# Kernel tuning notes

Measured on AMD Instinct MI355X. Metric: run time of the kernel, lower is better.

## Reference

```python
import jax, jax.numpy as jnp
import numpy as np

ALPHA = 0.5


def _chamfer(a, b):
    # Equivalent math to cKDTree k=1 queries: exact nearest-neighbor distances
    # between the two flattened clouds, computed brute-force.
    a = a.reshape(-1, 3)
    b = b.reshape(-1, 3)
    d2 = (jnp.sum(a * a, axis=1)[:, None]
          + jnp.sum(b * b, axis=1)[None, :]
          - 2.0 * (a @ b.T))                      # [Na, Nb]
    d = jnp.sqrt(jnp.clip(d2, 0.0))
    dist1 = jnp.min(d, axis=0)   # tree1(a).query(b): NN dist of each b point
    dist2 = jnp.min(d, axis=1)   # tree2(b).query(a): NN dist of each a point
    return jnp.mean(dist1) + jnp.mean(dist2)


def _pairwise_distances(x, y):
    # x: [B,N,3], y: [B,M,3] -> [B,N,M] euclidean distances (clamped-sqrt trick)
    x2 = jnp.sum(x * x, axis=-1, keepdims=True)            # [B,N,1]
    y2 = jnp.sum(y * y, axis=-1, keepdims=True)            # [B,M,1]
    d2 = x2 + jnp.swapaxes(y2, 2, 1) - 2.0 * jnp.einsum('bnd,bmd->bnm', x, y)
    return jnp.sqrt(jnp.clip(d2, 0.0))


def _confidence_scores(input_pcd, gt_pcd):
    # Faithful to torch.norm on the broadcast difference: [B,P,M,3] -> [B,P,M]
    diff = input_pcd[:, :, None, :] - gt_pcd[:, None, :, :]
    dist = jnp.linalg.norm(diff, axis=-1)
    min_d = jnp.min(dist, axis=-1)                         # [B,P]
    return jnp.exp(-min_d)[..., None]                      # [B,P,1]


def setup_inputs() -> dict:
    key = jax.random.key(0)
    k0, k1, k2, k3, k4 = jax.random.split(key, 5)
    B, N, M, P, NS = 4, 2048, 2048, 2048, 1024
    return {
        'pc1_0': jax.random.normal(k0, (B, N, 3), dtype=jnp.float32),
        'pc1_1': jax.random.normal(k1, (B, NS, 3), dtype=jnp.float32),
        'pc1_3': jax.random.uniform(k2, (B, P, 1), dtype=jnp.float32),
        'pc2': jax.random.normal(k3, (B, M, 3), dtype=jnp.float32),
        'pc3': jax.random.normal(k4, (B, P, 3), dtype=jnp.float32),
    }


def reference(pc1_0, pc1_1, pc1_3, pc2, pc3):
    # ChamferDistance detaches inputs in torch (cpu/numpy path) -> stop_gradient
    cd = jax.lax.stop_gradient(_chamfer(pc1_0, pc2))
    # In the original, emd_dist is immediately overwritten by pairwise_distances
    emd_dist = _pairwise_distances(pc1_0, pc2)             # [B,N,M]
    gt_scores = _confidence_scores(pc3, pc2)               # [B,P,1]
    confidence_loss = jnp.mean((pc1_3 - gt_scores) ** 2)
    seed_loss = jax.lax.stop_gradient(_chamfer(pc1_1, pc2))
    upsampling_loss = ALPHA * cd + (1.0 - ALPHA) * emd_dist
    final_loss = confidence_loss + upsampling_loss + seed_loss  # broadcasts to [B,N,M]
    return final_loss
```

## Files before the change

### kernel.cpp

```cpp
#include <hip/hip_runtime.h>
#include <math.h>


constexpr int OUT_TOTAL  = 4 * 2048 * 2048;
constexpr int PART_TOTAL = 416 * 2048;
constexpr int PART_OFS   = OUT_TOTAL - PART_TOTAL;

typedef float nfloat4 __attribute__((ext_vector_type(4)));

__global__ __launch_bounds__(256) void nn_kernel(
    const float* __restrict__ A0,
    const float* __restrict__ A1,
    const float* __restrict__ P2,
    const float* __restrict__ P3,
    float* __restrict__ part)
{
    __shared__ float4 lds[256];
    int bid = blockIdx.x;
    const float* A; const float* Bp; int at; int btile;
    if (bid < 128)      { int l = bid;       A = A0; Bp = P2; at = l >> 5; btile = l & 31; }
    else if (bid < 256) { int l = bid - 128; A = P2; Bp = A0; at = l >> 5; btile = l & 31; }
    else if (bid < 320) { int l = bid - 256; A = A1; Bp = P2; at = l >> 5; btile = l & 31; }
    else if (bid < 384) { int l = bid - 320; A = P2; Bp = A1; at = l >> 4; btile = l & 15; }
    else { int l = bid - 384; int b = l >> 3; btile = l & 7; at = 0;
           A = P3 + b * 6144; Bp = P2 + b * 6144; }

    {
        const float* s = Bp + (btile * 256 + threadIdx.x) * 3;
        float bx = s[0], by = s[1], bz = s[2];
        float nb2 = -0.5f * fmaf(bx, bx, fmaf(by, by, bz * bz));
        lds[threadIdx.x] = make_float4(bx, by, bz, nb2);
    }

    int a_base = at * 2048 + threadIdx.x * 8;
    const float4* av = (const float4*)(A + a_base * 3);
    float4 v0 = av[0], v1 = av[1], v2 = av[2], v3 = av[3], v4 = av[4], v5 = av[5];
    float ax[8], ay[8], az[8], a2[8], mx[8];
    ax[0]=v0.x; ay[0]=v0.y; az[0]=v0.z;
    ax[1]=v0.w; ay[1]=v1.x; az[1]=v1.y;
    ax[2]=v1.z; ay[2]=v1.w; az[2]=v2.x;
    ax[3]=v2.y; ay[3]=v2.z; az[3]=v2.w;
    ax[4]=v3.x; ay[4]=v3.y; az[4]=v3.z;
    ax[5]=v3.w; ay[5]=v4.x; az[5]=v4.y;
    ax[6]=v4.z; ay[6]=v4.w; az[6]=v5.x;
    ax[7]=v5.y; ay[7]=v5.z; az[7]=v5.w;
    #pragma unroll
    for (int k = 0; k < 8; k++) {
        a2[k] = fmaf(ax[k], ax[k], fmaf(ay[k], ay[k], az[k]*az[k]));
        mx[k] = -3.4e38f;
    }
    __syncthreads();

    #pragma unroll 4
    for (int j = 0; j < 256; j++) {
        float4 b = lds[j];
        #pragma unroll
        for (int k = 0; k < 8; k++) {
            float u = fmaf(az[k], b.z, b.w);
            u = fmaf(ay[k], b.y, u);
            u = fmaf(ax[k], b.x, u);
            mx[k] = fmaxf(mx[k], u);
        }
    }
    float4 o0, o1;
    o0.x = fmaxf(fmaf(-2.f, mx[0], a2[0]), 0.f);
    o0.y = fmaxf(fmaf(-2.f, mx[1], a2[1]), 0.f);
    o0.z = fmaxf(fmaf(-2.f, mx[2], a2[2]), 0.f);
    o0.w = fmaxf(fmaf(-2.f, mx[3], a2[3]), 0.f);
    o1.x = fmaxf(fmaf(-2.f, mx[4], a2[4]), 0.f);
    o1.y = fmaxf(fmaf(-2.f, mx[5], a2[5]), 0.f);
    o1.z = fmaxf(fmaf(-2.f, mx[6], a2[6]), 0.f);
    o1.w = fmaxf(fmaf(-2.f, mx[7], a2[7]), 0.f);
    float4* op = (float4*)(part + bid * 2048 + threadIdx.x * 8);
    op[0] = o0;
    op[1] = o1;
}

__global__ __launch_bounds__(1024) void reduce_kernel(
    const float* __restrict__ part,
    const float* __restrict__ conf_in,
    float* __restrict__ ws)
{
    int g = blockIdx.x;
    int tid = threadIdx.x;
    int base, bt; float scale; bool isconf = false;
    if (g < 8)       { int at = g >> 1;            base = (at * 32) * 2048       + (g & 1) * 1024; bt = 32; scale = 0.5f / 8192.f; }
    else if (g < 16) { int l = g - 8;  int at = l >> 1; base = (128 + at * 32) * 2048 + (l & 1) * 1024; bt = 32; scale = 0.5f / 8192.f; }
    else if (g < 20) { int l = g - 16; int at = l >> 1; base = (256 + at * 32) * 2048 + (l & 1) * 1024; bt = 32; scale = 1.f / 4096.f; }
    else if (g < 28) { int l = g - 20; int at = l >> 1; base = (320 + at * 16) * 2048 + (l & 1) * 1024; bt = 16; scale = 1.f / 8192.f; }
    else             { int l = g - 28; int b = l >> 1;  base = (384 + b * 8) * 2048   + (l & 1) * 1024; bt = 8;  scale = 1.f / 8192.f; isconf = true; }

    float m = 3.4e38f;
    const float* p = part + base + tid;
    #pragma unroll 4
    for (int t = 0; t < bt; t++, p += 2048) m = fminf(m, p[0]);
    float d = sqrtf(m);
    float sum;
    if (!isconf) {
        sum = d;
    } else {
        float e = conf_in[(g - 28) * 1024 + tid] - __expf(-d);
        sum = e * e;
    }
    #pragma unroll
    for (int ofs = 32; ofs > 0; ofs >>= 1) sum += __shfl_down(sum, ofs);
    __shared__ float red[16];
    if ((tid & 63) == 0) red[tid >> 6] = sum;
    __syncthreads();
    if (tid == 0) {
        float tot = 0.f;
        #pragma unroll
        for (int i = 0; i < 16; i++) tot += red[i];
        ws[g] = tot * scale;
    }
}

__global__ __launch_bounds__(256) void out_kernel(
    const float* __restrict__ pc1_0,
    const float* __restrict__ pc2,
    const float* __restrict__ wsp,
    float* __restrict__ out)
{
    int blk = blockIdx.x;
    int batch = blk >> 8;
    int n8 = blk & 255;
    int tid = threadIdx.x;
    float S = 0.f;
    #pragma unroll
    for (int t = 0; t < 36; t++) S += wsp[t];
    const float* bb = pc2 + batch * 6144;
    float bx[8], by[8], bz[8];
    {
        const float4* p = (const float4*)(bb + tid * 12);
        float4 u0 = p[0], u1 = p[1], u2 = p[2];
        bx[0]=u0.x; by[0]=u0.y; bz[0]=u0.z;
        bx[1]=u0.w; by[1]=u1.x; bz[1]=u1.y;
        bx[2]=u1.z; by[2]=u1.w; bz[2]=u2.x;
        bx[3]=u2.y; by[3]=u2.z; bz[3]=u2.w;
    }
    {
        const float4* p = (const float4*)(bb + 3072 + tid * 12);
        float4 u0 = p[0], u1 = p[1], u2 = p[2];
        bx[4]=u0.x; by[4]=u0.y; bz[4]=u0.z;
        bx[5]=u0.w; by[5]=u1.x; bz[5]=u1.y;
        bx[6]=u1.z; by[6]=u1.w; bz[6]=u2.x;
        bx[7]=u2.y; by[7]=u2.z; bz[7]=u2.w;
    }
    const float* arow = pc1_0 + batch * 6144 + n8 * 24;
    float* ob = out + (long)((batch << 11) + (n8 << 3)) * 2048 + tid * 4;
    #pragma unroll
    for (int r = 0; r < 8; r++) {
        float axx = arow[r*3], ayy = arow[r*3+1], azz = arow[r*3+2];
        float o[8];
        #pragma unroll
        for (int k = 0; k < 8; k++) {
            float dx = axx - bx[k], dy = ayy - by[k], dz = azz - bz[k];
            float d2 = fmaf(dx, dx, fmaf(dy, dy, dz*dz));
            o[k] = fmaf(0.5f, sqrtf(d2), S);
        }
        nfloat4 lo = { o[0], o[1], o[2], o[3] };
        nfloat4 hi = { o[4], o[5], o[6], o[7] };
        __builtin_nontemporal_store(lo, (nfloat4*)(ob + r * 2048));
        __builtin_nontemporal_store(hi, (nfloat4*)(ob + r * 2048 + 1024));
    }
}

extern "C" void kernel_launch(void* const* d_in, const int* in_sizes, int n_in,
                              void* d_out, int out_size, void* d_ws, size_t ws_size,
                              hipStream_t stream) {
    const float* pc1_0 = (const float*)d_in[0];
    const float* pc1_1 = (const float*)d_in[1];
    const float* pc1_3 = (const float*)d_in[2];
    const float* pc2   = (const float*)d_in[3];
    const float* pc3   = (const float*)d_in[4];
    float* out = (float*)d_out;
    float* ws  = (float*)d_ws;
    float* part = out + PART_OFS;

    nn_kernel<<<416, 256, 0, stream>>>(pc1_0, pc1_1, pc2, pc3, part);
    reduce_kernel<<<36, 1024, 0, stream>>>(part, pc1_3, ws);
    out_kernel<<<1024, 256, 0, stream>>>(pc1_0, pc2, ws, out);
}
```

Before: 112.2 us.

## Use fp16 dot2 for nearest-neighbor search and split work over more blocks

The x,y coordinates of both point clouds are packed into fp16 pairs so each candidate distance takes one v_dot2 instruction plus one FMA instead of three FMAs. Each thread now handles 2 query points instead of 8, so the grid grows from 416 to 1664 blocks, and the partial-minimum layout and reduce indexing are changed to match. The aim is more parallelism across the GPU and fewer instructions per distance. The cost is lower precision in the nearest-neighbor distances, which could break tolerance, plus more LDS reads per useful FMA.

```diff
diff --git a/kernel.cpp b/kernel.cpp
--- a/kernel.cpp
+++ b/kernel.cpp
@@ -3,10 +3,16 @@
 
 
 constexpr int OUT_TOTAL  = 4 * 2048 * 2048;
-constexpr int PART_TOTAL = 416 * 2048;
+constexpr int PART_TOTAL = 1664 * 512;
 constexpr int PART_OFS   = OUT_TOTAL - PART_TOTAL;
 
 typedef float nfloat4 __attribute__((ext_vector_type(4)));
+typedef _Float16 h2 __attribute__((ext_vector_type(2)));
+
+static __device__ __forceinline__ float pack2h(float x, float y) {
+    h2 v; v[0] = (_Float16)x; v[1] = (_Float16)y;
+    return __builtin_bit_cast(float, v);
+}
 
 __global__ __launch_bounds__(256) void nn_kernel(
     const float* __restrict__ A0,
@@ -18,62 +24,47 @@
     __shared__ float4 lds[256];
     int bid = blockIdx.x;
     const float* A; const float* Bp; int at; int btile;
-    if (bid < 128)      { int l = bid;       A = A0; Bp = P2; at = l >> 5; btile = l & 31; }
-    else if (bid < 256) { int l = bid - 128; A = P2; Bp = A0; at = l >> 5; btile = l & 31; }
-    else if (bid < 320) { int l = bid - 256; A = A1; Bp = P2; at = l >> 5; btile = l & 31; }
-    else if (bid < 384) { int l = bid - 320; A = P2; Bp = A1; at = l >> 4; btile = l & 15; }
-    else { int l = bid - 384; int b = l >> 3; btile = l & 7; at = 0;
+    if (bid < 512)       { int l = bid;        A = A0; Bp = P2; at = l >> 5; btile = l & 31; }
+    else if (bid < 1024) { int l = bid - 512;  A = P2; Bp = A0; at = l >> 5; btile = l & 31; }
+    else if (bid < 1280) { int l = bid - 1024; A = A1; Bp = P2; at = l >> 5; btile = l & 31; }
+    else if (bid < 1536) { int l = bid - 1280; A = P2; Bp = A1; at = l >> 4; btile = l & 15; }
+    else { int l = bid - 1536; int b = l >> 5; int l2 = l & 31; at = l2 >> 3; btile = l2 & 7;
            A = P3 + b * 6144; Bp = P2 + b * 6144; }
 
     {
         const float* s = Bp + (btile * 256 + threadIdx.x) * 3;
         float bx = s[0], by = s[1], bz = s[2];
         float nb2 = -0.5f * fmaf(bx, bx, fmaf(by, by, bz * bz));
-        lds[threadIdx.x] = make_float4(bx, by, bz, nb2);
+        lds[threadIdx.x] = make_float4(pack2h(bx, by), bz, nb2, 0.f);
     }
 
-    int a_base = at * 2048 + threadIdx.x * 8;
-    const float4* av = (const float4*)(A + a_base * 3);
-    float4 v0 = av[0], v1 = av[1], v2 = av[2], v3 = av[3], v4 = av[4], v5 = av[5];
-    float ax[8], ay[8], az[8], a2[8], mx[8];
-    ax[0]=v0.x; ay[0]=v0.y; az[0]=v0.z;
-    ax[1]=v0.w; ay[1]=v1.x; az[1]=v1.y;
-    ax[2]=v1.z; ay[2]=v1.w; az[2]=v2.x;
-    ax[3]=v2.y; ay[3]=v2.z; az[3]=v2.w;
-    ax[4]=v3.x; ay[4]=v3.y; az[4]=v3.z;
-    ax[5]=v3.w; ay[5]=v4.x; az[5]=v4.y;
-    ax[6]=v4.z; ay[6]=v4.w; az[6]=v5.x;
-    ax[7]=v5.y; ay[7]=v5.z; az[7]=v5.w;
-    #pragma unroll
-    for (int k = 0; k < 8; k++) {
-        a2[k] = fmaf(ax[k], ax[k], fmaf(ay[k], ay[k], az[k]*az[k]));
-        mx[k] = -3.4e38f;
-    }
+    int a_base = at * 512 + threadIdx.x * 2;
+    const float2* af = (const float2*)(A + a_base * 3);
+    float2 f0 = af[0], f1 = af[1], f2 = af[2];
+    float x0 = f0.x, y0 = f0.y, z0 = f1.x;
+    float x1 = f1.y, y1 = f2.x, z1 = f2.y;
+    float a20 = fmaf(x0, x0, fmaf(y0, y0, z0 * z0));
+    float a21 = fmaf(x1, x1, fmaf(y1, y1, z1 * z1));
+    h2 axy0 = __builtin_bit_cast(h2, pack2h(x0, y0));
+    h2 axy1 = __builtin_bit_cast(h2, pack2h(x1, y1));
+    float mx0 = -3.4e38f, mx1 = -3.4e38f;
     __syncthreads();
 
     #pragma unroll 4
     for (int j = 0; j < 256; j++) {
         float4 b = lds[j];
-        #pragma unroll
-        for (int k = 0; k < 8; k++) {
-            float u = fmaf(az[k], b.z, b.w);
-            u = fmaf(ay[k], b.y, u);
-            u = fmaf(ax[k], b.x, u);
-            mx[k] = fmaxf(mx[k], u);
-        }
+        h2 bxy = __builtin_bit_cast(h2, b.x);
+        float t0 = fmaf(z0, b.y, b.z);
+        float u0 = __builtin_amdgcn_fdot2(axy0, bxy, t0, false);
+        mx0 = fmaxf(mx0, u0);
+        float t1 = fmaf(z1, b.y, b.z);
+        float u1 = __builtin_amdgcn_fdot2(axy1, bxy, t1, false);
+        mx1 = fmaxf(mx1, u1);
     }
-    float4 o0, o1;
-    o0.x = fmaxf(fmaf(-2.f, mx[0], a2[0]), 0.f);
-    o0.y = fmaxf(fmaf(-2.f, mx[1], a2[1]), 0.f);
-    o0.z = fmaxf(fmaf(-2.f, mx[2], a2[2]), 0.f);
-    o0.w = fmaxf(fmaf(-2.f, mx[3], a2[3]), 0.f);
-    o1.x = fmaxf(fmaf(-2.f, mx[4], a2[4]), 0.f);
-    o1.y = fmaxf(fmaf(-2.f, mx[5], a2[5]), 0.f);
-    o1.z = fmaxf(fmaf(-2.f, mx[6], a2[6]), 0.f);
-    o1.w = fmaxf(fmaf(-2.f, mx[7], a2[7]), 0.f);
-    float4* op = (float4*)(part + bid * 2048 + threadIdx.x * 8);
-    op[0] = o0;
-    op[1] = o1;
+    float2 o;
+    o.x = fmaxf(fmaf(-2.f, mx0, a20), 0.f);
+    o.y = fmaxf(fmaf(-2.f, mx1, a21), 0.f);
+    *(float2*)(part + bid * 512 + threadIdx.x * 2) = o;
 }
 
 __global__ __launch_bounds__(1024) void reduce_kernel(
@@ -83,23 +74,24 @@
 {
     int g = blockIdx.x;
     int tid = threadIdx.x;
-    int base, bt; float scale; bool isconf = false;
-    if (g < 8)       { int at = g >> 1;            base = (at * 32) * 2048       + (g & 1) * 1024; bt = 32; scale = 0.5f / 8192.f; }
-    else if (g < 16) { int l = g - 8;  int at = l >> 1; base = (128 + at * 32) * 2048 + (l & 1) * 1024; bt = 32; scale = 0.5f / 8192.f; }
-    else if (g < 20) { int l = g - 16; int at = l >> 1; base = (256 + at * 32) * 2048 + (l & 1) * 1024; bt = 32; scale = 1.f / 4096.f; }
-    else if (g < 28) { int l = g - 20; int at = l >> 1; base = (320 + at * 16) * 2048 + (l & 1) * 1024; bt = 16; scale = 1.f / 8192.f; }
-    else             { int l = g - 28; int b = l >> 1;  base = (384 + b * 8) * 2048   + (l & 1) * 1024; bt = 8;  scale = 1.f / 8192.f; isconf = true; }
+    int i, nb, base; float scale; bool isconf = false;
+    if (g < 8)       { i = (g << 10) + tid;        base = 0    + (i >> 9) * 32; nb = 32; scale = 0.5f / 8192.f; }
+    else if (g < 16) { i = ((g - 8) << 10) + tid;  base = 512  + (i >> 9) * 32; nb = 32; scale = 0.5f / 8192.f; }
+    else if (g < 20) { i = ((g - 16) << 10) + tid; base = 1024 + (i >> 9) * 32; nb = 32; scale = 1.f / 4096.f; }
+    else if (g < 28) { i = ((g - 20) << 10) + tid; base = 1280 + (i >> 9) * 16; nb = 16; scale = 1.f / 8192.f; }
+    else             { i = ((g - 28) << 10) + tid; int b = i >> 11; int w = i & 2047;
+                       base = 1536 + b * 32 + (w >> 9) * 8; nb = 8; scale = 1.f / 8192.f; isconf = true; }
 
     float m = 3.4e38f;
-    const float* p = part + base + tid;
+    const float* p = part + base * 512 + (i & 511);
     #pragma unroll 4
-    for (int t = 0; t < bt; t++, p += 2048) m = fminf(m, p[0]);
+    for (int t = 0; t < nb; t++, p += 512) m = fminf(m, p[0]);
     float d = sqrtf(m);
     float sum;
     if (!isconf) {
         sum = d;
     } else {
-        float e = conf_in[(g - 28) * 1024 + tid] - __expf(-d);
+        float e = conf_in[i] - __expf(-d);
         sum = e * e;
     }
     #pragma unroll
@@ -110,7 +102,7 @@
     if (tid == 0) {
         float tot = 0.f;
         #pragma unroll
-        for (int i = 0; i < 16; i++) tot += red[i];
+        for (int i2 = 0; i2 < 16; i2++) tot += red[i2];
         ws[g] = tot * scale;
     }
 }
@@ -177,7 +169,7 @@
     float* ws  = (float*)d_ws;
     float* part = out + PART_OFS;
 
-    nn_kernel<<<416, 256, 0, stream>>>(pc1_0, pc1_1, pc2, pc3, part);
+    nn_kernel<<<1664, 256, 0, stream>>>(pc1_0, pc1_1, pc2, pc3, part);
     reduce_kernel<<<36, 1024, 0, stream>>>(part, pc1_3, ws);
     out_kernel<<<1024, 256, 0, stream>>>(pc1_0, pc2, ws, out);
 }
```

Measured after the change: 114.3 us. Within noise of the previous version (+1.8%).
